# Kernel optimization log

Measured on AMD Instinct MI355X. Metric: run time of the kernel, lower is better.

## Reference

```python
import jax, jax.numpy as jnp
import numpy as np
import math

DIM_EMB = 1024
DIM_QK = 1024
DIM_V = 1024
NORM_FACT = 1.0 / math.sqrt(DIM_EMB)

def setup_inputs() -> dict:
    key = jax.random.key(0)
    k0, k1, k2, k3 = jax.random.split(key, 4)
    x = jax.random.normal(k0, (4, 4096, DIM_EMB), dtype=jnp.float32)
    # nn.Linear weights are [out_features, in_features]; y = x @ W.T
    s = 1.0 / math.sqrt(DIM_EMB)
    Wq = jax.random.uniform(k1, (DIM_QK, DIM_EMB), jnp.float32, -s, s)
    Wk = jax.random.uniform(k2, (DIM_QK, DIM_EMB), jnp.float32, -s, s)
    Wv = jax.random.uniform(k3, (DIM_V, DIM_EMB), jnp.float32, -s, s)
    return {"x": x, "Wq": Wq, "Wk": Wk, "Wv": Wv}

def reference(x, Wq, Wk, Wv):
    # q,k,v: [b, n, d]
    q = jnp.einsum('bne,de->bnd', x, Wq)
    k = jnp.einsum('bne,de->bnd', x, Wk)
    v = jnp.einsum('bne,de->bnd', x, Wv)
    logits = jnp.einsum('bnd,bmd->bnm', q, k)  # [b, n, n]
    # Faithful to source: softmax over last dim FIRST, then scale by 1/sqrt(dim_embedding)
    score = jax.nn.softmax(logits, axis=-1) * NORM_FACT
    att = jnp.einsum('bnm,bmv->bnv', score, v)
    return att
```

## Files before the change

### kernel.cpp

```cpp
#include <hip/hip_runtime.h>
#include <hip/hip_bf16.h>

typedef _Float16 f16;
typedef _Float16 f16x4 __attribute__((ext_vector_type(4)));
typedef _Float16 f16x8 __attribute__((ext_vector_type(8)));
typedef float f32x4 __attribute__((ext_vector_type(4)));

__device__ __forceinline__ void gload16(const void* g, void* l) {
    __builtin_amdgcn_global_load_lds(
        (const __attribute__((address_space(1))) void*)g,
        (__attribute__((address_space(3))) void*)l, 16, 0, 0);
}

#define FENCE asm volatile("" ::: "memory")
#define BARRIER do { FENCE; __builtin_amdgcn_s_barrier(); FENCE; } while (0)

#define PHASE_MFMA(QI, QJ)                                                    \
    __builtin_amdgcn_s_setprio(1);                                            \
    _Pragma("unroll")                                                         \
    for (int ks = 0; ks < 2; ++ks)                                            \
      _Pragma("unroll")                                                       \
      for (int i = 0; i < 4; ++i)                                             \
        _Pragma("unroll")                                                     \
        for (int j = 0; j < 2; ++j)                                           \
          acc[(QI)*4 + i][(QJ)*2 + j] = __builtin_amdgcn_mfma_f32_16x16x32_f16( \
              a[i][ks], b[j][ks], acc[(QI)*4 + i][(QJ)*2 + j], 0, 0, 0);      \
    __builtin_amdgcn_s_setprio(0);

#define BT8_BODY(KBASE, NTILES)                                               \
    const int rr8 = lane >> 3;                                                \
    const int cs  = ((lane & 7) ^ rr8) << 3;                                  \
    const int ldsr = wid << 3;                                                \
    auto stageA = [&](int kt, int c, int h) {                                 \
        const size_t g0 = (size_t)(bm + (h << 7) + ldsr + rr8) * lda + (KBASE) + kt + cs; \
        gload16(A + g0,                      &sA[c][((h << 7) + ldsr) << 6]); \
        gload16(A + g0 + ((size_t)lda << 6), &sA[c][((h << 7) + 64 + ldsr) << 6]); \
    };                                                                        \
    auto stageB = [&](int kt, int c, int h) {                                 \
        const size_t g0 = (size_t)(bn + (h << 7) + ldsr + rr8) * ldb + (KBASE) + kt + cs; \
        gload16(B + g0,                      &sB[c][((h << 7) + ldsr) << 6]); \
        gload16(B + g0 + ((size_t)ldb << 6), &sB[c][((h << 7) + 64 + ldsr) << 6]); \
    };                                                                        \
    f32x4 acc[8][4] = {};                                                     \
    f16x8 a[4][2], b[2][2];                                                   \
    auto loadA = [&](int c, int qi) {                                         \
        _Pragma("unroll")                                                     \
        for (int i = 0; i < 4; ++i) {                                         \
            const int ra = wr * 128 + (qi * 4 + i) * 16 + (lane & 15);        \
            const int swz = (ra & 7) << 3;                                    \
            _Pragma("unroll")                                                 \
            for (int ks = 0; ks < 2; ++ks) {                                  \
                const int kk = ks * 32 + (lane >> 4) * 8;                     \
                a[i][ks] = *(const f16x8*)(&sA[c][(ra << 6) + (kk ^ swz)]);   \
            }                                                                 \
        }                                                                     \
    };                                                                        \
    auto loadB = [&](int c, int qj) {                                         \
        _Pragma("unroll")                                                     \
        for (int j = 0; j < 2; ++j) {                                         \
            const int rb = wc * 64 + (qj * 2 + j) * 16 + (lane & 15);         \
            const int swz = (rb & 7) << 3;                                    \
            _Pragma("unroll")                                                 \
            for (int ks = 0; ks < 2; ++ks) {                                  \
                const int kk = ks * 32 + (lane >> 4) * 8;                     \
                b[j][ks] = *(const f16x8*)(&sB[c][(rb << 6) + (kk ^ swz)]);   \
            }                                                                 \
        }                                                                     \
    };                                                                        \
    stageA(0, 0, 0); stageA(0, 0, 1); stageB(0, 0, 0); stageB(0, 0, 1);       \
    asm volatile("s_waitcnt vmcnt(0)" ::: "memory");                          \
    BARRIER;                                                                  \
    for (int g = 0; g < (NTILES); ++g) {                                      \
        const int c = g & 1, cn = c ^ 1;                                      \
        const int kn = (g + 1) << 6;                                          \
        const bool more = (g + 1) < (NTILES);                                 \
        loadA(c, 0); loadB(c, 0);                                             \
        if (more) { stageA(kn, cn, 0); stageA(kn, cn, 1); }                   \
        BARRIER; PHASE_MFMA(0, 0); BARRIER;                                   \
        loadB(c, 1);                                                          \
        if (more) { stageB(kn, cn, 0); stageB(kn, cn, 1); }                   \
        BARRIER; PHASE_MFMA(0, 1); BARRIER;                                   \
        loadA(c, 1); loadB(c, 0);                                             \
        BARRIER; PHASE_MFMA(1, 0); BARRIER;                                   \
        loadB(c, 1);                                                          \
        asm volatile("s_waitcnt vmcnt(0)" ::: "memory");                      \
        BARRIER; PHASE_MFMA(1, 1); BARRIER;                                   \
    }

template<bool F16OUT>
__global__ __launch_bounds__(512) void gemm_bt8(
    const f16* __restrict__ A, const f16* __restrict__ B, void* __restrict__ Cv,
    int K, int lda, int ldb, int ldc, float scale, int nbn)
{
    __shared__ f16 sA[2][256 * 64];
    __shared__ f16 sB[2][256 * 64];
    const int tid = threadIdx.x, lane = tid & 63, wid = tid >> 6;
    const int wr = wid >> 2, wc = wid & 3;
    const int cpx = gridDim.x >> 3;
    const int wg = (blockIdx.x & 7) * cpx + (blockIdx.x >> 3);
    const int bm = (wg / nbn) << 8, bn = (wg % nbn) << 8;

    BT8_BODY(0, K >> 6)

#pragma unroll
    for (int i = 0; i < 8; ++i)
#pragma unroll
        for (int j = 0; j < 4; ++j)
#pragma unroll
            for (int r = 0; r < 4; ++r) {
                const int row = bm + wr * 128 + i * 16 + ((lane >> 4) << 2) + r;
                const int col = bn + wc * 64 + j * 16 + (lane & 15);
                if constexpr (F16OUT)
                    ((f16*)Cv)[(size_t)row * ldc + col] = (f16)(acc[i][j][r] * scale);
                else
                    ((float*)Cv)[(size_t)row * ldc + col] = acc[i][j][r] * scale;
            }
}

__global__ __launch_bounds__(512) void gemm_qk(
    const f16* __restrict__ A, const f16* __restrict__ B,
    f16* __restrict__ S, int lda, int ldb)
{
    __shared__ f16 sA[2][256 * 64];
    __shared__ f16 sB[2][256 * 64];
    const int tid = threadIdx.x, lane = tid & 63, wid = tid >> 6;
    const int wr = wid >> 2, wc = wid & 3;
    const int cpx = gridDim.x >> 3;
    const int wg = (blockIdx.x & 7) * cpx + (blockIdx.x >> 3);
    const int bm = (wg >> 4) << 8, bn = (wg & 15) << 8;

    BT8_BODY(0, 16)

    {
        f16* Tb = wr ? (f16*)sB : (f16*)sA;
        const int lg = lane >> 4;
#pragma unroll
        for (int i = 0; i < 8; ++i)
#pragma unroll
            for (int j = 0; j < 4; ++j)
#pragma unroll
                for (int r = 0; r < 4; ++r) {
                    const int rloc = i * 16 + lg * 4 + r;
                    const int col  = wc * 64 + j * 16 + (lane & 15);
                    Tb[rloc * 256 + (col ^ (((rloc >> 2) & 7) << 3))] = (f16)acc[i][j][r];
                }
    }
    BARRIER;
#pragma unroll
    for (int u = 0; u < 16; ++u) {
        const int gi = u * 512 + tid;
        const int row = gi >> 5;
        const int c0 = (gi & 31) << 3;
        const f16* Tb = (row & 128) ? (const f16*)sB : (const f16*)sA;
        f16x8 v = *(const f16x8*)(Tb + (row & 127) * 256
                                  + (c0 ^ (((row >> 2) & 7) << 3)));
        *(f16x8*)(S + (size_t)(bm + row) * 4096 + bn + c0) = v;
    }
}

__global__ __launch_bounds__(256) void softmax_f16(f16* S)
{
    const int lane = threadIdx.x & 63, wid = threadIdx.x >> 6;
    const int row = blockIdx.x * 4 + wid;
    f16* src = S + (size_t)row * 4096;
    f16x8 v[8];
#pragma unroll
    for (int u = 0; u < 8; ++u) v[u] = *(const f16x8*)(src + u * 512 + lane * 8);
    float m = -1e30f;
#pragma unroll
    for (int u = 0; u < 8; ++u)
#pragma unroll
        for (int e = 0; e < 8; ++e) m = fmaxf(m, (float)v[u][e]);
#pragma unroll
    for (int msk = 1; msk <= 32; msk <<= 1) m = fmaxf(m, __shfl_xor(m, msk));
    float ev[64];
    float s = 0.f;
#pragma unroll
    for (int u = 0; u < 8; ++u)
#pragma unroll
        for (int e = 0; e < 8; ++e) {
            const float x = __expf((float)v[u][e] - m);
            ev[u * 8 + e] = x; s += x;
        }
#pragma unroll
    for (int msk = 1; msk <= 32; msk <<= 1) s += __shfl_xor(s, msk);
    const float inv = 1.0f / (32.0f * s);
#pragma unroll
    for (int u = 0; u < 8; ++u) {
        f16x8 p;
#pragma unroll
        for (int e = 0; e < 8; ++e) p[e] = (f16)(ev[u * 8 + e] * inv);
        *(f16x8*)(src + u * 512 + lane * 8) = p;
    }
}

__global__ __launch_bounds__(512) void gemm_pv8(
    const f16* __restrict__ A, const f16* __restrict__ B, float* __restrict__ Cout,
    f16* __restrict__ Pp, int lda, int ldb)
{
    __shared__ f16 sA[2][256 * 64];
    __shared__ f16 sB[2][256 * 64];
    const int tid = threadIdx.x, lane = tid & 63, wid = tid >> 6;
    const int wr = wid >> 2, wc = wid & 3;
    const int cpx = gridDim.x >> 3;
    const int wg = (blockIdx.x & 7) * cpx + (blockIdx.x >> 3);
    const int bm = (wg >> 2) << 8, bn = (wg & 3) << 8;
    const int z = blockIdx.y;
    const int kbase = z << 10;

    BT8_BODY(kbase, 16)

#pragma unroll
    for (int i = 0; i < 8; ++i)
#pragma unroll
        for (int j = 0; j < 4; ++j)
#pragma unroll
            for (int r = 0; r < 4; ++r) {
                const int row = bm + wr * 128 + i * 16 + ((lane >> 4) << 2) + r;
                const int col = bn + wc * 64 + j * 16 + (lane & 15);
                const float v = acc[i][j][r];
                if (z == 3)
                    Cout[((size_t)row << 10) + col] = v;
                else
                    Pp[(size_t)z * 4194304 + ((size_t)row << 10) + col] = (f16)v;
            }
}

__global__ __launch_bounds__(256) void reduce_pv(
    float* __restrict__ Cout, const f16* __restrict__ Pp)
{
    const int i = blockIdx.x * 256 + threadIdx.x;
    const int r = i >> 7;
    const int c = (i & 127) << 3;
    const size_t base = ((size_t)r << 10) + c;
    const f16x8 p0 = *(const f16x8*)(Pp + base);
    const f16x8 p1 = *(const f16x8*)(Pp + base + 4194304);
    const f16x8 p2 = *(const f16x8*)(Pp + base + 8388608);
    float* o = Cout + base;
    float4 o0 = *(float4*)o, o1 = *(float4*)(o + 4);
    o0.x += (float)p0[0] + (float)p1[0] + (float)p2[0];
    o0.y += (float)p0[1] + (float)p1[1] + (float)p2[1];
    o0.z += (float)p0[2] + (float)p1[2] + (float)p2[2];
    o0.w += (float)p0[3] + (float)p1[3] + (float)p2[3];
    o1.x += (float)p0[4] + (float)p1[4] + (float)p2[4];
    o1.y += (float)p0[5] + (float)p1[5] + (float)p2[5];
    o1.z += (float)p0[6] + (float)p1[6] + (float)p2[6];
    o1.w += (float)p0[7] + (float)p1[7] + (float)p2[7];
    *(float4*)o = o0;
    *(float4*)(o + 4) = o1;
}

__global__ __launch_bounds__(256) void gemm_vt(
    const f16* __restrict__ A, const f16* __restrict__ B, f16* __restrict__ C,
    int K, int lda, int ldb, int ldc)
{
    __shared__ f16 sA[2][128 * 64];
    __shared__ f16 sB[2][128 * 64];
    const int tid = threadIdx.x, lane = tid & 63, wid = tid >> 6;
    const int wr = wid >> 1, wc = wid & 1;
    const int bm = blockIdx.x * 128, bn = blockIdx.y * 128;

    f32x4 acc[4][4] = {};

    auto stage16 = [&](int kt, int bsel) {
        const int rsub = lane >> 3;
        const int csw = ((lane & 7) ^ rsub) << 3;
#pragma unroll
        for (int i = 0; i < 4; ++i) {
            const int rb = (wid * 4 + i) * 8;
            gload16(A + (size_t)(bm + rb + rsub) * lda + kt + csw, &sA[bsel][rb * 64]);
            gload16(B + (size_t)(bn + rb + rsub) * ldb + kt + csw, &sB[bsel][rb * 64]);
        }
    };

    auto compute = [&](int bsel) {
#pragma unroll
        for (int ks = 0; ks < 2; ++ks) {
            const int kk = ks * 32 + (lane >> 4) * 8;
            f16x8 a[4], b[4];
#pragma unroll
            for (int i = 0; i < 4; ++i) {
                const int ra = wr * 64 + i * 16 + (lane & 15);
                a[i] = *(const f16x8*)(&sA[bsel][(ra << 6) + (kk ^ ((ra & 7) << 3))]);
                const int rb2 = wc * 64 + i * 16 + (lane & 15);
                b[i] = *(const f16x8*)(&sB[bsel][(rb2 << 6) + (kk ^ ((rb2 & 7) << 3))]);
            }
#pragma unroll
            for (int i = 0; i < 4; ++i)
#pragma unroll
                for (int j = 0; j < 4; ++j)
                    acc[i][j] = __builtin_amdgcn_mfma_f32_16x16x32_f16(a[i], b[j], acc[i][j], 0, 0, 0);
        }
    };

    stage16(0, 0);
    asm volatile("s_waitcnt vmcnt(0)" ::: "memory");
    __syncthreads();
    const int NT2 = K >> 6;
    for (int t = 0; t < NT2; ++t) {
        if (t + 1 < NT2) stage16((t + 1) << 6, (t + 1) & 1);
        compute(t & 1);
        asm volatile("s_waitcnt vmcnt(0)" ::: "memory");
        __builtin_amdgcn_s_barrier();
    }
#pragma unroll
    for (int i = 0; i < 4; ++i)
#pragma unroll
        for (int j = 0; j < 4; ++j)
#pragma unroll
            for (int r = 0; r < 4; ++r) {
                const int row = bm + wr * 64 + i * 16 + (lane >> 4) * 4 + r;
                const int col = bn + wc * 64 + j * 16 + (lane & 15);
                C[(size_t)row * ldc + col] = (f16)acc[i][j][r];
            }
}

__global__ __launch_bounds__(256) void cvt3(
    const float* __restrict__ x, const float* __restrict__ wq, const float* __restrict__ wk,
    f16* __restrict__ dx, f16* __restrict__ dwq, f16* __restrict__ dwk)
{
    const int i = blockIdx.x * 256 + threadIdx.x;
    const float* s; f16* d; int off;
    if (i < 2097152)      { s = x;  d = dx;  off = i; }
    else if (i < 2228224) { s = wq; d = dwq; off = i - 2097152; }
    else                  { s = wk; d = dwk; off = i - 2228224; }
    const float4 a = ((const float4*)s)[off * 2];
    const float4 b = ((const float4*)s)[off * 2 + 1];
    f16x8 o = { (f16)a.x, (f16)a.y, (f16)a.z, (f16)a.w,
                (f16)b.x, (f16)b.y, (f16)b.z, (f16)b.w };
    ((f16x8*)d)[off] = o;
}

__global__ __launch_bounds__(256) void cvt_batch(
    const float* __restrict__ xb, const float* __restrict__ wv,
    f16* __restrict__ dxb, f16* __restrict__ dwv)
{
    const int i = blockIdx.x * 256 + threadIdx.x;
    const float* s; f16* d; int off;
    if (i < 524288) { s = xb; d = dxb; off = i; }
    else            { s = wv; d = dwv; off = i - 524288; }
    const float4 a = ((const float4*)s)[off * 2];
    const float4 b = ((const float4*)s)[off * 2 + 1];
    f16x8 o = { (f16)a.x, (f16)a.y, (f16)a.z, (f16)a.w,
                (f16)b.x, (f16)b.y, (f16)b.z, (f16)b.w };
    ((f16x8*)d)[off] = o;
}

extern "C" void kernel_launch(void* const* d_in, const int* in_sizes, int n_in,
                              void* d_out, int out_size, void* d_ws, size_t ws_size,
                              hipStream_t stream) {
    const float* x  = (const float*)d_in[0];
    const float* Wq = (const float*)d_in[1];
    const float* Wk = (const float*)d_in[2];
    const float* Wv = (const float*)d_in[3];
    float* out = (float*)d_out;

    f16*   qk  = (f16*)d_out;
    f16*   xh  = (f16*)d_ws;
    f16*   wqh = (f16*)((char*)d_ws + (32LL << 20));
    f16*   wkh = wqh + 1024LL * 1024;

    f16*   S   = (f16*)d_ws;
    f16*   Pp  = (f16*)((char*)d_ws + (32LL << 20));
    f16*   vTw = (f16*)((char*)d_ws + (56LL << 20));

    cvt3<<<9216, 256, 0, stream>>>(x, Wq, Wk, xh, wqh, wkh);

    gemm_bt8<true><<<256, 512, 0, stream>>>(xh, wqh, qk,        1024, 1024, 1024, 2048, 1.f, 4);
    gemm_bt8<true><<<256, 512, 0, stream>>>(xh, wkh, qk + 1024, 1024, 1024, 1024, 2048, 1.f, 4);

    for (int b = 0; b < 4; ++b) {
        const size_t tb = (size_t)b * 4096;
        f16* xhb = (f16*)(out + tb * 1024);
        f16* wvh = xhb + 4096LL * 1024;
        gemm_qk<<<256, 512, 0, stream>>>(
            qk + tb * 2048, qk + tb * 2048 + 1024, S, 2048, 2048);
        softmax_f16<<<1024, 256, 0, stream>>>(S);
        cvt_batch<<<2560, 256, 0, stream>>>(x + tb * 1024, Wv, xhb, wvh);
        gemm_vt<<<dim3(8, 32), 256, 0, stream>>>(wvh, xhb, vTw, 1024, 1024, 1024, 4096);
        gemm_pv8<<<dim3(64, 4), 512, 0, stream>>>(S, vTw, out + tb * 1024, Pp, 4096, 4096);
        reduce_pv<<<2048, 256, 0, stream>>>(out + tb * 1024, Pp);
    }
}
```

Baseline: 565.5 us.

## Replace four-phase barrier-interleaved GEMM loop with per-k-slice load-then-MFMA schedule

```diff
diff --git a/kernel.cpp b/kernel.cpp
--- a/kernel.cpp
+++ b/kernel.cpp
@@ -14,18 +14,6 @@
 
 #define FENCE asm volatile("" ::: "memory")
 #define BARRIER do { FENCE; __builtin_amdgcn_s_barrier(); FENCE; } while (0)
-
-#define PHASE_MFMA(QI, QJ)                                                    \
-    __builtin_amdgcn_s_setprio(1);                                            \
-    _Pragma("unroll")                                                         \
-    for (int ks = 0; ks < 2; ++ks)                                            \
-      _Pragma("unroll")                                                       \
-      for (int i = 0; i < 4; ++i)                                             \
-        _Pragma("unroll")                                                     \
-        for (int j = 0; j < 2; ++j)                                           \
-          acc[(QI)*4 + i][(QJ)*2 + j] = __builtin_amdgcn_mfma_f32_16x16x32_f16( \
-              a[i][ks], b[j][ks], acc[(QI)*4 + i][(QJ)*2 + j], 0, 0, 0);      \
-    __builtin_amdgcn_s_setprio(0);
 
 #define BT8_BODY(KBASE, NTILES)                                               \
     const int rr8 = lane >> 3;                                                \
@@ -42,31 +30,6 @@
         gload16(B + g0 + ((size_t)ldb << 6), &sB[c][((h << 7) + 64 + ldsr) << 6]); \
     };                                                                        \
     f32x4 acc[8][4] = {};                                                     \
-    f16x8 a[4][2], b[2][2];                                                   \
-    auto loadA = [&](int c, int qi) {                                         \
-        _Pragma("unroll")                                                     \
-        for (int i = 0; i < 4; ++i) {                                         \
-            const int ra = wr * 128 + (qi * 4 + i) * 16 + (lane & 15);        \
-            const int swz = (ra & 7) << 3;                                    \
-            _Pragma("unroll")                                                 \
-            for (int ks = 0; ks < 2; ++ks) {                                  \
-                const int kk = ks * 32 + (lane >> 4) * 8;                     \
-                a[i][ks] = *(const f16x8*)(&sA[c][(ra << 6) + (kk ^ swz)]);   \
-            }                                                                 \
-        }                                                                     \
-    };                                                                        \
-    auto loadB = [&](int c, int qj) {                                         \
-        _Pragma("unroll")                                                     \
-        for (int j = 0; j < 2; ++j) {                                         \
-            const int rb = wc * 64 + (qj * 2 + j) * 16 + (lane & 15);         \
-            const int swz = (rb & 7) << 3;                                    \
-            _Pragma("unroll")                                                 \
-            for (int ks = 0; ks < 2; ++ks) {                                  \
-                const int kk = ks * 32 + (lane >> 4) * 8;                     \
-                b[j][ks] = *(const f16x8*)(&sB[c][(rb << 6) + (kk ^ swz)]);   \
-            }                                                                 \
-        }                                                                     \
-    };                                                                        \
     stageA(0, 0, 0); stageA(0, 0, 1); stageB(0, 0, 0); stageB(0, 0, 1);       \
     asm volatile("s_waitcnt vmcnt(0)" ::: "memory");                          \
     BARRIER;                                                                  \
@@ -74,17 +37,33 @@
         const int c = g & 1, cn = c ^ 1;                                      \
         const int kn = (g + 1) << 6;                                          \
         const bool more = (g + 1) < (NTILES);                                 \
-        loadA(c, 0); loadB(c, 0);                                             \
-        if (more) { stageA(kn, cn, 0); stageA(kn, cn, 1); }                   \
-        BARRIER; PHASE_MFMA(0, 0); BARRIER;                                   \
-        loadB(c, 1);                                                          \
-        if (more) { stageB(kn, cn, 0); stageB(kn, cn, 1); }                   \
-        BARRIER; PHASE_MFMA(0, 1); BARRIER;                                   \
-        loadA(c, 1); loadB(c, 0);                                             \
-        BARRIER; PHASE_MFMA(1, 0); BARRIER;                                   \
-        loadB(c, 1);                                                          \
+        if (more) { stageA(kn, cn, 0); stageA(kn, cn, 1);                     \
+                    stageB(kn, cn, 0); stageB(kn, cn, 1); }                   \
+        _Pragma("unroll")                                                     \
+        for (int ks = 0; ks < 2; ++ks) {                                      \
+            f16x8 a[8], b[4];                                                 \
+            const int kk = ks * 32 + ((lane >> 4) << 3);                      \
+            _Pragma("unroll")                                                 \
+            for (int i = 0; i < 8; ++i) {                                     \
+                const int ra = wr * 128 + i * 16 + (lane & 15);               \
+                a[i] = *(const f16x8*)(&sA[c][(ra << 6) + (kk ^ ((ra & 7) << 3))]); \
+            }                                                                 \
+            _Pragma("unroll")                                                 \
+            for (int j = 0; j < 4; ++j) {                                     \
+                const int rb = wc * 64 + j * 16 + (lane & 15);                \
+                b[j] = *(const f16x8*)(&sB[c][(rb << 6) + (kk ^ ((rb & 7) << 3))]); \
+            }                                                                 \
+            __builtin_amdgcn_s_setprio(1);                                    \
+            _Pragma("unroll")                                                 \
+            for (int i = 0; i < 8; ++i)                                       \
+                _Pragma("unroll")                                             \
+                for (int j = 0; j < 4; ++j)                                   \
+                    acc[i][j] = __builtin_amdgcn_mfma_f32_16x16x32_f16(       \
+                        a[i], b[j], acc[i][j], 0, 0, 0);                      \
+            __builtin_amdgcn_s_setprio(0);                                    \
+        }                                                                     \
         asm volatile("s_waitcnt vmcnt(0)" ::: "memory");                      \
-        BARRIER; PHASE_MFMA(1, 1); BARRIER;                                   \
+        BARRIER;                                                              \
     }
 
 template<bool F16OUT>
```

After: 582.2 us. 2.9% more time.
